# Optimization experiments

Measured on AMD Instinct MI355X. Metric: run time of the kernel, lower is better.

The kernel has to match this reference:

```python
import jax, jax.numpy as jnp
import numpy as np

IN_F, OUT_F = 1024, 1024
GRID_SIZE, SPLINE_ORDER = 5, 3
BATCH = 4096


def _make_grid():
    # grid_range = [-1, 1], h = 2 / grid_size
    h = 2.0 / GRID_SIZE
    g = jnp.arange(-SPLINE_ORDER, GRID_SIZE + SPLINE_ORDER + 1, dtype=jnp.float32) * h - 1.0
    return jnp.broadcast_to(g, (IN_F, g.shape[0]))  # [in, 12]


def setup_inputs() -> dict:
    key = jax.random.key(0)
    k1, k2, k3, k4 = jax.random.split(key, 4)
    x = jax.random.normal(k1, (BATCH, IN_F), dtype=jnp.float32) * 0.5
    base_weight = jax.random.normal(k2, (OUT_F, IN_F), dtype=jnp.float32) * (1.0 / np.sqrt(IN_F))
    # matches reset_parameters noise scale: (rand-0.5)*0.1/grid_size
    spline_weight = (jax.random.uniform(k3, (OUT_F, IN_F, GRID_SIZE + SPLINE_ORDER)) - 0.5) * (0.1 / GRID_SIZE)
    spline_scaler = jax.random.normal(k4, (OUT_F, IN_F), dtype=jnp.float32) * (1.0 / np.sqrt(IN_F))
    return {"x": x, "base_weight": base_weight, "spline_weight": spline_weight,
            "spline_scaler": spline_scaler, "grid": _make_grid()}


def _b_splines(x, grid):
    # x: [B, F], grid: [F, G]; returns [B, F, grid_size + spline_order]
    xe = x[..., None]  # [B, F, 1]
    bases = ((xe >= grid[:, :-1]) & (xe < grid[:, 1:])).astype(x.dtype)  # [B,F,G-1]
    for k in range(1, SPLINE_ORDER + 1):
        left = (xe - grid[:, : -(k + 1)]) / (grid[:, k:-1] - grid[:, : -(k + 1)])
        right = (grid[:, k + 1 :] - xe) / (grid[:, k + 1 :] - grid[:, 1:-k])
        bases = left * bases[:, :, :-1] + right * bases[:, :, 1:]
    return bases


def reference(x, base_weight, spline_weight, spline_scaler, grid):
    base_out = jax.nn.silu(x) @ base_weight.T  # [B, out]
    basis = _b_splines(x, grid)  # [B, in, 8]
    scaled_w = spline_weight * spline_scaler[..., None]  # [out, in, 8]
    spline_out = jnp.einsum('bfi,ofi->bo', basis, scaled_w)
    return base_out + spline_out
```

## Files before the change

### kernel.cpp

```cpp
#include <hip/hip_runtime.h>
#include <hip/hip_bf16.h>

#define IN_F   1024
#define OUT_F  1024
#define GS     5
#define SO     3
#define NB     (GS + SO)
#define NG     (GS + 2*SO + 1)
#define BATCH  4096
#define KC     (IN_F + IN_F * NB)
#define BM 256
#define BN 256
#define BK 64
#define SPLITK 4
#define KPART  (KC / SPLITK)
#define NT     (KPART / BK)

typedef __bf16 bf16x8 __attribute__((ext_vector_type(8)));
typedef float  f32x4  __attribute__((ext_vector_type(4)));

__device__ __forceinline__ void gload_lds16(const void* g, void* l) {
    __builtin_amdgcn_global_load_lds(
        (const __attribute__((address_space(1))) void*)g,
        (__attribute__((address_space(3))) void*)l,
        16, 0, 0);
}

#define WC_BLK 4608
#define A_BLK  18432

__global__ __launch_bounds__(256) void prep_all(const float* __restrict__ bw,
                                                const float* __restrict__ sw,
                                                const float* __restrict__ ss,
                                                const float* __restrict__ x,
                                                __bf16* __restrict__ W,
                                                __bf16* __restrict__ A) {
    if (blockIdx.x < WC_BLK) {
        const int t = blockIdx.x * 256 + threadIdx.x;
        const int NBASE = OUT_F * IN_F / 8;
        if (t < NBASE) {
            const int o  = t >> 7;
            const int c8 = (t & 127) * 8;
            const float4* sp = (const float4*)(bw + (size_t)o * IN_F + c8);
            float4 v0 = sp[0], v1 = sp[1];
            float v[8] = {v0.x, v0.y, v0.z, v0.w, v1.x, v1.y, v1.z, v1.w};
            bf16x8 ov;
#pragma unroll
            for (int j = 0; j < 8; ++j) ov[j] = (__bf16)v[j];
            *(bf16x8*)(W + (size_t)o * KC + c8) = ov;
        } else {
            const int u = t - NBASE;
            if (u >= OUT_F * IN_F) return;
            const int o = u >> 10, f = u & 1023;
            const float s = ss[(size_t)o * IN_F + f];
            const float4* sp = (const float4*)(sw + ((size_t)o * IN_F + f) * NB);
            float4 v0 = sp[0], v1 = sp[1];
            float v[8] = {v0.x, v0.y, v0.z, v0.w, v1.x, v1.y, v1.z, v1.w};
            bf16x8 ov;
#pragma unroll
            for (int j = 0; j < 8; ++j) ov[j] = (__bf16)(v[j] * s);
            *(bf16x8*)(W + (size_t)o * KC + IN_F + (size_t)f * NB) = ov;
        }
    } else {
        const int t = (blockIdx.x - WC_BLK) * 256 + threadIdx.x;
        const int NBASE = BATCH * IN_F / 8;
        if (t < NBASE) {
            const int b  = t >> 7;
            const int c8 = (t & 127) * 8;
            const float4* sp = (const float4*)(x + (size_t)b * IN_F + c8);
            float4 v0 = sp[0], v1 = sp[1];
            float v[8] = {v0.x, v0.y, v0.z, v0.w, v1.x, v1.y, v1.z, v1.w};
            bf16x8 ov;
#pragma unroll
            for (int j = 0; j < 8; ++j) {
                float xx = v[j];
                ov[j] = (__bf16)(xx / (1.0f + __expf(-xx)));
            }
            *(bf16x8*)(A + (size_t)b * KC + c8) = ov;
        } else {
            const int u = t - NBASE;
            if (u >= BATCH * IN_F) return;
            const int b = u >> 10, f = u & 1023;
            const float xv = x[(size_t)b * IN_F + f];
            const float h = 2.0f / GS;
            float gv[NG];
#pragma unroll
            for (int j = 0; j < NG; ++j) gv[j] = (float)(j - SO) * h - 1.0f;
            float bas[NB + SO];
#pragma unroll
            for (int j = 0; j < NB + SO; ++j)
                bas[j] = (xv >= gv[j] && xv < gv[j + 1]) ? 1.0f : 0.0f;
#pragma unroll
            for (int k = 1; k <= SO; ++k) {
                const float rk = 1.0f / ((float)k * h);
#pragma unroll
                for (int j = 0; j <= (NB + SO - 1) - k; ++j) {
                    float left  = (xv - gv[j]) * rk;
                    float right = (gv[j + k + 1] - xv) * rk;
                    bas[j] = left * bas[j] + right * bas[j + 1];
                }
            }
            bf16x8 ov;
#pragma unroll
            for (int i = 0; i < NB; ++i) ov[i] = (__bf16)bas[i];
            *(bf16x8*)(A + (size_t)b * KC + IN_F + (size_t)f * NB) = ov;
        }
    }
}

__global__ __launch_bounds__(256) void zero_out(float4* __restrict__ p, int n4) {
    const int i = blockIdx.x * 256 + threadIdx.x;
    if (i < n4) p[i] = float4{0.f, 0.f, 0.f, 0.f};
}

__global__ __launch_bounds__(256) void reduce_k(float4* __restrict__ C,
                                                const float4* __restrict__ P) {
    const size_t n4 = (size_t)BATCH * OUT_F / 4;
    for (size_t i = blockIdx.x * 256 + threadIdx.x; i < n4; i += 2048 * 256) {
        float4 c  = C[i];
        float4 p0 = P[i];
        float4 p1 = P[n4 + i];
        float4 p2 = P[2 * n4 + i];
        c.x += p0.x + p1.x + p2.x;
        c.y += p0.y + p1.y + p2.y;
        c.z += p0.z + p1.z + p2.z;
        c.w += p0.w + p1.w + p2.w;
        C[i] = c;
    }
}

#define PH_SYNC do { __builtin_amdgcn_s_barrier();                            \
    asm volatile("s_waitcnt lgkmcnt(0)" ::: "memory");                        \
    __builtin_amdgcn_sched_barrier(0); } while (0)

#define MFMA16(AF, BF, MI0, NI0)                                              \
    __builtin_amdgcn_s_setprio(1);                                            \
    _Pragma("unroll")                                                         \
    for (int kk_ = 0; kk_ < 2; ++kk_)                                         \
        _Pragma("unroll")                                                     \
        for (int i_ = 0; i_ < 4; ++i_)                                        \
            _Pragma("unroll")                                                 \
            for (int n_ = 0; n_ < 2; ++n_)                                    \
                acc[(MI0) + i_][(NI0) + n_] =                                 \
                    __builtin_amdgcn_mfma_f32_16x16x32_bf16(                  \
                        AF[i_][kk_], BF[n_][kk_],                             \
                        acc[(MI0) + i_][(NI0) + n_], 0, 0, 0);                \
    __builtin_amdgcn_s_setprio(0);                                            \
    __builtin_amdgcn_s_barrier();

#define RD_A4(DST, LBUF, MI0)                                                 \
    _Pragma("unroll")                                                         \
    for (int i_ = 0; i_ < 4; ++i_) {                                          \
        DST[i_][0] = *(const bf16x8*)&(LBUF)[((MI0) + i_) * 1024 + aRow + slot0]; \
        DST[i_][1] = *(const bf16x8*)&(LBUF)[((MI0) + i_) * 1024 + aRow + slot1]; \
    }

#define RD_B2(DST, LBUF, NI0)                                                 \
    _Pragma("unroll")                                                         \
    for (int n_ = 0; n_ < 2; ++n_) {                                          \
        DST[n_][0] = *(const bf16x8*)&(LBUF)[bRow + ((NI0) + n_) * 1024 + slot0]; \
        DST[n_][1] = *(const bf16x8*)&(LBUF)[bRow + ((NI0) + n_) * 1024 + slot1]; \
    }

template<bool ATOMIC>
__global__ __launch_bounds__(512, 2) void kan_gemm(const __bf16* __restrict__ A,
                                                   const __bf16* __restrict__ W,
                                                   float* __restrict__ C,
                                                   float* __restrict__ P) {
    __shared__ __bf16 sA[2][2][128 * BK];
    __shared__ __bf16 sB[2][2][128 * BK];

    const int tid  = threadIdx.x;
    const int gid  = blockIdx.x;
    const int work = (gid & 7) * 32 + (gid >> 3);
    const int ks = work >> 6;
    const int bn = (work >> 4) & 3;
    const int bm = work & 15;

    const int lane = tid & 63;
    const int wv   = tid >> 6;
    const int wm   = wv >> 2;
    const int wn   = wv & 3;
    const int lr   = lane & 15;
    const int hi   = lane >> 4;
    const int key  = lr & 7;

    const int slot0 = ((hi ^ key) << 3);
    const int slot1 = (((4 + hi) ^ key) << 3);
    const int aRow  = lr * 64;
    const int bRow  = ((wn & 1) * 64 + lr) * 64;

    const int srow = tid >> 3;
    const int scol = ((tid & 7) ^ (srow & 7)) << 3;

    const __bf16* gA = A + (size_t)(bm * BM) * KC + ks * KPART;
    const __bf16* gW = W + (size_t)(bn * BN) * KC + ks * KPART;

    f32x4 acc[8][4] = {};
    bf16x8 a0[4][2], a1[4][2], b01[2][2], b23[2][2];

    auto stageA = [&](int buf, int h, int kt) {
#pragma unroll
        for (int l = 0; l < 2; ++l)
            gload_lds16(gA + (size_t)(h * 128 + l * 64 + srow) * KC + kt * BK + scol,
                        &sA[buf][h][(l * 512 + tid) * 8]);
    };
    auto stageB = [&](int buf, int h, int kt) {
#pragma unroll
        for (int l = 0; l < 2; ++l)
            gload_lds16(gW + (size_t)(h * 128 + l * 64 + srow) * KC + kt * BK + scol,
                        &sB[buf][h][(l * 512 + tid) * 8]);
    };

    stageA(0, 0, 0); stageA(0, 1, 0); stageB(0, 0, 0); stageB(0, 1, 0);
    stageA(1, 0, 1); stageA(1, 1, 1); stageB(1, 0, 1);
    asm volatile("s_waitcnt vmcnt(6)\n\ts_barrier" ::: "memory");

    for (int kt = 0; kt < NT; ++kt) {
        const int b = kt & 1;
        const __bf16* LA = &sA[b][wm][0];
        const __bf16* LB = &sB[b][wn >> 1][0];

        RD_A4(a0, LA, 0);
        RD_B2(b01, LB, 0);
        PH_SYNC;
        MFMA16(a0, b01, 0, 0);

        RD_B2(b23, LB, 2);
        if (kt + 1 < NT) stageB(b ^ 1, 1, kt + 1);
        PH_SYNC;
        MFMA16(a0, b23, 0, 2);

        RD_A4(a1, LA, 4);
        if (kt + 2 < NT) stageB(b, 0, kt + 2);
        PH_SYNC;
        MFMA16(a1, b01, 4, 0);

        if (kt + 2 < NT) { stageA(b, 0, kt + 2); stageA(b, 1, kt + 2); }
        __builtin_amdgcn_s_barrier();
        __builtin_amdgcn_s_setprio(1);
#pragma unroll
        for (int kk_ = 0; kk_ < 2; ++kk_)
#pragma unroll
            for (int i_ = 0; i_ < 4; ++i_)
#pragma unroll
                for (int n_ = 0; n_ < 2; ++n_)
                    acc[4 + i_][2 + n_] = __builtin_amdgcn_mfma_f32_16x16x32_bf16(
                        a1[i_][kk_], b23[n_][kk_], acc[4 + i_][2 + n_], 0, 0, 0);
        __builtin_amdgcn_s_setprio(0);

        if (kt + 2 < NT)
            asm volatile("s_waitcnt vmcnt(6)\n\ts_barrier" ::: "memory");
        else if (kt + 1 < NT)
            asm volatile("s_waitcnt vmcnt(0)\n\ts_barrier" ::: "memory");
    }

    const int cr = hi * 4, cc = lane & 15;
    float* dst;
    if (ATOMIC) dst = C;
    else        dst = (ks == 0) ? C : P + (size_t)(ks - 1) * BATCH * OUT_F;
#pragma unroll
    for (int mi = 0; mi < 8; ++mi)
#pragma unroll
        for (int ni = 0; ni < 4; ++ni) {
            float* cp = dst + (size_t)(bm * BM + wm * 128 + mi * 16 + cr) * OUT_F
                            + bn * BN + wn * 64 + ni * 16 + cc;
#pragma unroll
            for (int r = 0; r < 4; ++r) {
                if (ATOMIC) unsafeAtomicAdd(cp + (size_t)r * OUT_F, acc[mi][ni][r]);
                else        cp[(size_t)r * OUT_F] = acc[mi][ni][r];
            }
        }
}

extern "C" void kernel_launch(void* const* d_in, const int* in_sizes, int n_in,
                              void* d_out, int out_size, void* d_ws, size_t ws_size,
                              hipStream_t stream) {
    const float* x    = (const float*)d_in[0];
    const float* bw   = (const float*)d_in[1];
    const float* sw   = (const float*)d_in[2];
    const float* ss   = (const float*)d_in[3];

    const size_t wc_bytes   = (size_t)OUT_F * KC * 2;
    const size_t a_bytes    = (size_t)BATCH * KC * 2;
    const size_t part_bytes = 3ull * BATCH * OUT_F * 4;
    if (ws_size < wc_bytes + a_bytes) return;

    __bf16* Wc = (__bf16*)d_ws;
    __bf16* A  = (__bf16*)((char*)d_ws + wc_bytes);
    float*  P  = (float*)((char*)d_ws + wc_bytes + a_bytes);

    prep_all<<<WC_BLK + A_BLK, 256, 0, stream>>>(bw, sw, ss, x, Wc, A);

    const int grid = (BATCH / BM) * (OUT_F / BN) * SPLITK;
    if (ws_size >= wc_bytes + a_bytes + part_bytes) {
        kan_gemm<false><<<grid, 512, 0, stream>>>(A, Wc, (float*)d_out, P);
        reduce_k<<<2048, 256, 0, stream>>>((float4*)d_out, (const float4*)P);
    } else {
        const int n4 = BATCH * OUT_F / 4;
        zero_out<<<n4 / 256, 256, 0, stream>>>((float4*)d_out, n4);
        kan_gemm<true><<<grid, 512, 0, stream>>>(A, Wc, (float*)d_out, P);
    }
}
```

Baseline: 117.2 us.

## Switch GEMM to 128x128 tiles with 4 waves and split-K of 2

Shrinks the GEMM block tile from 256x256 with 8 waves to 128x128 with 4 waves, halves split-K from 4 to 2, and replaces the hand-phased staged pipeline with a simpler double-buffered loop that prefetches the next K tile before each MFMA pass. The reduce kernel and partial buffer shrink to match the single extra partial. The aim is less partial-sum traffic and reduce work, and more blocks for occupancy. The cost is lower per-block data reuse, which raises global/L2 load traffic, and a less finely interleaved load/compute schedule.

New measurement: 117.5 us. Within noise of the previous version (+0.2%).

```diff
diff --git a/kernel.cpp b/kernel.cpp
--- a/kernel.cpp
+++ b/kernel.cpp
@@ -9,10 +9,10 @@
 #define NG     (GS + 2*SO + 1)
 #define BATCH  4096
 #define KC     (IN_F + IN_F * NB)
-#define BM 256
-#define BN 256
+#define BM 128
+#define BN 128
 #define BK 64
-#define SPLITK 4
+#define SPLITK 2
 #define KPART  (KC / SPLITK)
 #define NT     (KPART / BK)
 
@@ -117,23 +117,13 @@
                                                 const float4* __restrict__ P) {
     const size_t n4 = (size_t)BATCH * OUT_F / 4;
     for (size_t i = blockIdx.x * 256 + threadIdx.x; i < n4; i += 2048 * 256) {
-        float4 c  = C[i];
-        float4 p0 = P[i];
-        float4 p1 = P[n4 + i];
-        float4 p2 = P[2 * n4 + i];
-        c.x += p0.x + p1.x + p2.x;
-        c.y += p0.y + p1.y + p2.y;
-        c.z += p0.z + p1.z + p2.z;
-        c.w += p0.w + p1.w + p2.w;
+        float4 c = C[i], p = P[i];
+        c.x += p.x; c.y += p.y; c.z += p.z; c.w += p.w;
         C[i] = c;
     }
 }
 
-#define PH_SYNC do { __builtin_amdgcn_s_barrier();                            \
-    asm volatile("s_waitcnt lgkmcnt(0)" ::: "memory");                        \
-    __builtin_amdgcn_sched_barrier(0); } while (0)
-
-#define MFMA16(AF, BF, MI0, NI0)                                              \
+#define MFMA_Q(AF, BF, NI0)                                                   \
     __builtin_amdgcn_s_setprio(1);                                            \
     _Pragma("unroll")                                                         \
     for (int kk_ = 0; kk_ < 2; ++kk_)                                         \
@@ -141,129 +131,112 @@
         for (int i_ = 0; i_ < 4; ++i_)                                        \
             _Pragma("unroll")                                                 \
             for (int n_ = 0; n_ < 2; ++n_)                                    \
-                acc[(MI0) + i_][(NI0) + n_] =                                 \
+                acc[i_][(NI0) + n_] =                                         \
                     __builtin_amdgcn_mfma_f32_16x16x32_bf16(                  \
-                        AF[i_][kk_], BF[n_][kk_],                             \
-                        acc[(MI0) + i_][(NI0) + n_], 0, 0, 0);                \
-    __builtin_amdgcn_s_setprio(0);                                            \
-    __builtin_amdgcn_s_barrier();
-
-#define RD_A4(DST, LBUF, MI0)                                                 \
-    _Pragma("unroll")                                                         \
-    for (int i_ = 0; i_ < 4; ++i_) {                                          \
-        DST[i_][0] = *(const bf16x8*)&(LBUF)[((MI0) + i_) * 1024 + aRow + slot0]; \
-        DST[i_][1] = *(const bf16x8*)&(LBUF)[((MI0) + i_) * 1024 + aRow + slot1]; \
-    }
-
-#define RD_B2(DST, LBUF, NI0)                                                 \
-    _Pragma("unroll")                                                         \
-    for (int n_ = 0; n_ < 2; ++n_) {                                          \
-        DST[n_][0] = *(const bf16x8*)&(LBUF)[bRow + ((NI0) + n_) * 1024 + slot0]; \
-        DST[n_][1] = *(const bf16x8*)&(LBUF)[bRow + ((NI0) + n_) * 1024 + slot1]; \
-    }
+                        AF[i_][kk_], BF[n_][kk_], acc[i_][(NI0) + n_],        \
+                        0, 0, 0);                                             \
+    __builtin_amdgcn_s_setprio(0);
+
+#define LGKM0_FENCE do {                                                      \
+    asm volatile("s_waitcnt lgkmcnt(0)" ::: "memory");                        \
+    __builtin_amdgcn_sched_barrier(0); } while (0)
 
 template<bool ATOMIC>
-__global__ __launch_bounds__(512, 2) void kan_gemm(const __bf16* __restrict__ A,
+__global__ __launch_bounds__(256, 2) void kan_gemm(const __bf16* __restrict__ A,
                                                    const __bf16* __restrict__ W,
                                                    float* __restrict__ C,
                                                    float* __restrict__ P) {
-    __shared__ __bf16 sA[2][2][128 * BK];
-    __shared__ __bf16 sB[2][2][128 * BK];
+    __shared__ __bf16 sA[2][BM * BK];
+    __shared__ __bf16 sB[2][BN * BK];
 
     const int tid  = threadIdx.x;
     const int gid  = blockIdx.x;
-    const int work = (gid & 7) * 32 + (gid >> 3);
-    const int ks = work >> 6;
-    const int bn = (work >> 4) & 3;
-    const int bm = work & 15;
+    const int work = (gid & 7) * 64 + (gid >> 3);
+    const int ks = work >> 8;
+    const int bn = (work >> 5) & 7;
+    const int bm = work & 31;
 
     const int lane = tid & 63;
     const int wv   = tid >> 6;
-    const int wm   = wv >> 2;
-    const int wn   = wv & 3;
+    const int wm   = wv >> 1;
+    const int wn   = wv & 1;
     const int lr   = lane & 15;
     const int hi   = lane >> 4;
     const int key  = lr & 7;
 
     const int slot0 = ((hi ^ key) << 3);
     const int slot1 = (((4 + hi) ^ key) << 3);
-    const int aRow  = lr * 64;
-    const int bRow  = ((wn & 1) * 64 + lr) * 64;
-
-    const int srow = tid >> 3;
-    const int scol = ((tid & 7) ^ (srow & 7)) << 3;
+    const int aBase = (wm * 64 + lr) * BK;
+    const int bBase = (wn * 64 + lr) * BK;
 
     const __bf16* gA = A + (size_t)(bm * BM) * KC + ks * KPART;
     const __bf16* gW = W + (size_t)(bn * BN) * KC + ks * KPART;
 
-    f32x4 acc[8][4] = {};
-    bf16x8 a0[4][2], a1[4][2], b01[2][2], b23[2][2];
-
-    auto stageA = [&](int buf, int h, int kt) {
-#pragma unroll
-        for (int l = 0; l < 2; ++l)
-            gload_lds16(gA + (size_t)(h * 128 + l * 64 + srow) * KC + kt * BK + scol,
-                        &sA[buf][h][(l * 512 + tid) * 8]);
+    f32x4 acc[4][4] = {};
+    bf16x8 af[4][2], bf01[2][2], bf23[2][2];
+
+    auto stage = [&](int buf, int kt) {
+#pragma unroll
+        for (int p = 0; p < 4; ++p) {
+            const int chunk = p * 256 + tid;
+            const int row = chunk >> 3, slot = chunk & 7;
+            const int col = (slot ^ (row & 7)) << 3;
+            gload_lds16(gA + (size_t)row * KC + kt * BK + col,
+                        &sA[buf][chunk * 8]);
+        }
+#pragma unroll
+        for (int p = 0; p < 4; ++p) {
+            const int chunk = p * 256 + tid;
+            const int row = chunk >> 3, slot = chunk & 7;
+            const int col = (slot ^ (row & 7)) << 3;
+            gload_lds16(gW + (size_t)row * KC + kt * BK + col,
+                        &sB[buf][chunk * 8]);
+        }
     };
-    auto stageB = [&](int buf, int h, int kt) {
-#pragma unroll
-        for (int l = 0; l < 2; ++l)
-            gload_lds16(gW + (size_t)(h * 128 + l * 64 + srow) * KC + kt * BK + scol,
-                        &sB[buf][h][(l * 512 + tid) * 8]);
-    };
-
-    stageA(0, 0, 0); stageA(0, 1, 0); stageB(0, 0, 0); stageB(0, 1, 0);
-    stageA(1, 0, 1); stageA(1, 1, 1); stageB(1, 0, 1);
-    asm volatile("s_waitcnt vmcnt(6)\n\ts_barrier" ::: "memory");
+
+    stage(0, 0);
+    asm volatile("s_waitcnt vmcnt(0)\n\ts_barrier" ::: "memory");
 
     for (int kt = 0; kt < NT; ++kt) {
         const int b = kt & 1;
-        const __bf16* LA = &sA[b][wm][0];
-        const __bf16* LB = &sB[b][wn >> 1][0];
-
-        RD_A4(a0, LA, 0);
-        RD_B2(b01, LB, 0);
-        PH_SYNC;
-        MFMA16(a0, b01, 0, 0);
-
-        RD_B2(b23, LB, 2);
-        if (kt + 1 < NT) stageB(b ^ 1, 1, kt + 1);
-        PH_SYNC;
-        MFMA16(a0, b23, 0, 2);
-
-        RD_A4(a1, LA, 4);
-        if (kt + 2 < NT) stageB(b, 0, kt + 2);
-        PH_SYNC;
-        MFMA16(a1, b01, 4, 0);
-
-        if (kt + 2 < NT) { stageA(b, 0, kt + 2); stageA(b, 1, kt + 2); }
-        __builtin_amdgcn_s_barrier();
-        __builtin_amdgcn_s_setprio(1);
-#pragma unroll
-        for (int kk_ = 0; kk_ < 2; ++kk_)
-#pragma unroll
-            for (int i_ = 0; i_ < 4; ++i_)
-#pragma unroll
-                for (int n_ = 0; n_ < 2; ++n_)
-                    acc[4 + i_][2 + n_] = __builtin_amdgcn_mfma_f32_16x16x32_bf16(
-                        a1[i_][kk_], b23[n_][kk_], acc[4 + i_][2 + n_], 0, 0, 0);
-        __builtin_amdgcn_s_setprio(0);
-
-        if (kt + 2 < NT)
-            asm volatile("s_waitcnt vmcnt(6)\n\ts_barrier" ::: "memory");
-        else if (kt + 1 < NT)
+        const __bf16* LA = &sA[b][0];
+        const __bf16* LB = &sB[b][0];
+
+#pragma unroll
+        for (int i_ = 0; i_ < 4; ++i_) {
+            af[i_][0] = *(const bf16x8*)&LA[aBase + i_ * (16 * BK) + slot0];
+            af[i_][1] = *(const bf16x8*)&LA[aBase + i_ * (16 * BK) + slot1];
+        }
+#pragma unroll
+        for (int n_ = 0; n_ < 2; ++n_) {
+            bf01[n_][0] = *(const bf16x8*)&LB[bBase + n_ * (16 * BK) + slot0];
+            bf01[n_][1] = *(const bf16x8*)&LB[bBase + n_ * (16 * BK) + slot1];
+        }
+        if (kt + 1 < NT) stage(b ^ 1, kt + 1);
+        LGKM0_FENCE;
+        MFMA_Q(af, bf01, 0);
+
+#pragma unroll
+        for (int n_ = 0; n_ < 2; ++n_) {
+            bf23[n_][0] = *(const bf16x8*)&LB[bBase + (n_ + 2) * (16 * BK) + slot0];
+            bf23[n_][1] = *(const bf16x8*)&LB[bBase + (n_ + 2) * (16 * BK) + slot1];
+        }
+        LGKM0_FENCE;
+        MFMA_Q(af, bf23, 2);
+
+        if (kt + 1 < NT)
             asm volatile("s_waitcnt vmcnt(0)\n\ts_barrier" ::: "memory");
     }
 
     const int cr = hi * 4, cc = lane & 15;
     float* dst;
     if (ATOMIC) dst = C;
-    else        dst = (ks == 0) ? C : P + (size_t)(ks - 1) * BATCH * OUT_F;
-#pragma unroll
-    for (int mi = 0; mi < 8; ++mi)
+    else        dst = (ks == 0) ? C : P;
+#pragma unroll
+    for (int mi = 0; mi < 4; ++mi)
 #pragma unroll
         for (int ni = 0; ni < 4; ++ni) {
-            float* cp = dst + (size_t)(bm * BM + wm * 128 + mi * 16 + cr) * OUT_F
+            float* cp = dst + (size_t)(bm * BM + wm * 64 + mi * 16 + cr) * OUT_F
                             + bn * BN + wn * 64 + ni * 16 + cc;
 #pragma unroll
             for (int r = 0; r < 4; ++r) {
@@ -283,22 +256,22 @@
 
     const size_t wc_bytes   = (size_t)OUT_F * KC * 2;
     const size_t a_bytes    = (size_t)BATCH * KC * 2;
-    const size_t part_bytes = 3ull * BATCH * OUT_F * 4;
+    const size_t part_bytes = (size_t)BATCH * OUT_F * 4;
     if (ws_size < wc_bytes + a_bytes) return;
 
     __bf16* Wc = (__bf16*)d_ws;
     __bf16* A  = (__bf16*)((char*)d_ws + wc_bytes);
     float*  P  = (float*)((char*)d_ws + wc_bytes + a_bytes);
 
-    prep_all<<<WC_BLK + A_BLK, 256, 0, stream>>>(bw, sw, ss, x, Wc, A);
+    prep_all<<<WC_BLK + A_BLK, 256, 0, stream>>>(bw, ss ? sw : sw, ss, x, Wc, A);
 
     const int grid = (BATCH / BM) * (OUT_F / BN) * SPLITK;
     if (ws_size >= wc_bytes + a_bytes + part_bytes) {
-        kan_gemm<false><<<grid, 512, 0, stream>>>(A, Wc, (float*)d_out, P);
+        kan_gemm<false><<<grid, 256, 0, stream>>>(A, Wc, (float*)d_out, P);
         reduce_k<<<2048, 256, 0, stream>>>((float4*)d_out, (const float4*)P);
     } else {
         const int n4 = BATCH * OUT_F / 4;
         zero_out<<<n4 / 256, 256, 0, stream>>>((float4*)d_out, n4);
-        kan_gemm<true><<<grid, 512, 0, stream>>>(A, Wc, (float*)d_out, P);
-    }
-}
+        kan_gemm<true><<<grid, 256, 0, stream>>>(A, Wc, (float*)d_out, P);
+    }
+}
```

## Overlap LDS fragment reads with MFMA using partial lgkmcnt waits and fewer barriers

Applied to the files above, without the earlier changes.

Reschedules the per-K-tile loop of the split-K GEMM so the LDS reads for later fragments are issued before earlier MFMA groups run. Partial `s_waitcnt lgkmcnt(N)` fences replace the full waits. The per-phase `s_barrier` after every MFMA quarter is dropped, leaving only the barriers needed before overwriting LDS buffers with the next async global-to-LDS stages. This aims to hide LDS latency behind matrix work and cut barrier stalls. It relies on lgkm counter ordering being exact and keeps more fragment registers live at once.

Result: faster. 113.9 us (-2.8%).

```diff
diff --git a/kernel.cpp b/kernel.cpp
--- a/kernel.cpp
+++ b/kernel.cpp
@@ -129,11 +129,7 @@
     }
 }
 
-#define PH_SYNC do { __builtin_amdgcn_s_barrier();                            \
-    asm volatile("s_waitcnt lgkmcnt(0)" ::: "memory");                        \
-    __builtin_amdgcn_sched_barrier(0); } while (0)
-
-#define MFMA16(AF, BF, MI0, NI0)                                              \
+#define MFMAQ(AF, BF, MI0, NI0)                                               \
     __builtin_amdgcn_s_setprio(1);                                            \
     _Pragma("unroll")                                                         \
     for (int kk_ = 0; kk_ < 2; ++kk_)                                         \
@@ -145,8 +141,7 @@
                     __builtin_amdgcn_mfma_f32_16x16x32_bf16(                  \
                         AF[i_][kk_], BF[n_][kk_],                             \
                         acc[(MI0) + i_][(NI0) + n_], 0, 0, 0);                \
-    __builtin_amdgcn_s_setprio(0);                                            \
-    __builtin_amdgcn_s_barrier();
+    __builtin_amdgcn_s_setprio(0);
 
 #define RD_A4(DST, LBUF, MI0)                                                 \
     _Pragma("unroll")                                                         \
@@ -161,6 +156,10 @@
         DST[n_][0] = *(const bf16x8*)&(LBUF)[bRow + ((NI0) + n_) * 1024 + slot0]; \
         DST[n_][1] = *(const bf16x8*)&(LBUF)[bRow + ((NI0) + n_) * 1024 + slot1]; \
     }
+
+#define LGKM_FENCE(N)                                                         \
+    asm volatile("s_waitcnt lgkmcnt(" #N ")" ::: "memory");                   \
+    __builtin_amdgcn_sched_barrier(0)
 
 template<bool ATOMIC>
 __global__ __launch_bounds__(512, 2) void kan_gemm(const __bf16* __restrict__ A,
@@ -223,31 +222,25 @@
 
         RD_A4(a0, LA, 0);
         RD_B2(b01, LB, 0);
-        PH_SYNC;
-        MFMA16(a0, b01, 0, 0);
+        __builtin_amdgcn_sched_barrier(0);
 
         RD_B2(b23, LB, 2);
+        LGKM_FENCE(4);
+        MFMAQ(a0, b01, 0, 0);
+
+        RD_A4(a1, LA, 4);
         if (kt + 1 < NT) stageB(b ^ 1, 1, kt + 1);
-        PH_SYNC;
-        MFMA16(a0, b23, 0, 2);
-
-        RD_A4(a1, LA, 4);
+        LGKM_FENCE(8);
+        __builtin_amdgcn_s_barrier();
+        MFMAQ(a0, b23, 0, 2);
+
         if (kt + 2 < NT) stageB(b, 0, kt + 2);
-        PH_SYNC;
-        MFMA16(a1, b01, 4, 0);
+        LGKM_FENCE(0);
+        __builtin_amdgcn_s_barrier();
+        MFMAQ(a1, b01, 4, 0);
 
         if (kt + 2 < NT) { stageA(b, 0, kt + 2); stageA(b, 1, kt + 2); }
-        __builtin_amdgcn_s_barrier();
-        __builtin_amdgcn_s_setprio(1);
-#pragma unroll
-        for (int kk_ = 0; kk_ < 2; ++kk_)
-#pragma unroll
-            for (int i_ = 0; i_ < 4; ++i_)
-#pragma unroll
-                for (int n_ = 0; n_ < 2; ++n_)
-                    acc[4 + i_][2 + n_] = __builtin_amdgcn_mfma_f32_16x16x32_bf16(
-                        a1[i_][kk_], b23[n_][kk_], acc[4 + i_][2 + n_], 0, 0, 0);
-        __builtin_amdgcn_s_setprio(0);
+        MFMAQ(a1, b23, 4, 2);
 
         if (kt + 2 < NT)
             asm volatile("s_waitcnt vmcnt(6)\n\ts_barrier" ::: "memory");
```
